# Kernel optimization log

Hardware: AMD Instinct MI355X
Metric: run time of the kernel (lower is better)

## Reference

```python
import jax, jax.numpy as jnp
import numpy as np

N = 50000   # nodes
E = 800000  # edges (avg degree 16)
H = 8       # num_heads
D = 16      # head_dim = hidden_size // num_heads = 128 // 8


def setup_inputs() -> dict:
    key = jax.random.key(0)
    k1, k2, k3, k4, k5 = jax.random.split(key, 5)
    q = jax.random.normal(k1, (N, D, H), dtype=jnp.float32)
    k = jax.random.normal(k2, (N, D, H), dtype=jnp.float32)
    v = jax.random.normal(k3, (N, D, H), dtype=jnp.float32)
    # COO adjacency: row = destination node of each edge, col = source node
    row = jnp.sort(jax.random.randint(k4, (E,), 0, N, dtype=jnp.int32))
    col = jax.random.randint(k5, (E,), 0, N, dtype=jnp.int32)
    return {"q": q, "k": k, "v": v, "row": row, "col": col}


def reference(q, k, v, row, col):
    # bsddmm: sampled dense-dense matmul -> per-edge, per-head attention logits
    # logits[e, h] = sum_d q[row[e], d, h] * k[col[e], d, h]
    logits = jnp.einsum('edh,edh->eh', q[row], k[col])  # [E, H]

    # sparse softmax over each destination row (per head), numerically stable
    m = jax.ops.segment_max(logits, row, num_segments=N)  # [N, H]
    p = jnp.exp(logits - m[row])                          # [E, H]
    s = jax.ops.segment_sum(p, row, num_segments=N)       # [N, H]
    attn = p / s[row]                                     # [E, H]

    # bspmm: out[i, d, h] = sum_{e: row[e]==i} attn[e, h] * v[col[e], d, h]
    out = jax.ops.segment_sum(attn[:, None, :] * v[col], row, num_segments=N)  # [N, D, H]
    return out.reshape(N, -1)  # [N, D*H]
```

## Files before the change

### kernel.cpp

```cpp
#include <hip/hip_runtime.h>
#include <math.h>

#define HEADS 8
#define DIM 16
#define NPB 32

__global__ __launch_bounds__(256) void spmha_kernel(
    const float* __restrict__ q, const float* __restrict__ k, const float* __restrict__ v,
    const int* __restrict__ row, const int* __restrict__ col,
    float* __restrict__ out, int N, int E) {
  __shared__ int rp[NPB + 1];

  int node0 = blockIdx.x * NPB;

  if (threadIdx.x <= NPB) {
    int target = node0 + threadIdx.x;
    int lo = 0, hi = E;
    while (lo < hi) {
      int mid = (lo + hi) >> 1;
      if (row[mid] < target) lo = mid + 1; else hi = mid;
    }
    rp[threadIdx.x] = lo;
  }
  __syncthreads();

  int il = threadIdx.x >> 3;
  int i  = node0 + il;
  int l  = threadIdx.x & 7;
  bool alive = (i < N);

  int s = alive ? rp[il] : 0;
  int e = alive ? rp[il + 1] : 0;

  float qv[16];
  if (alive) {
    const float4* qb = (const float4*)(q + (size_t)i * 128);
#pragma unroll
    for (int r = 0; r < 4; ++r) *(float4*)&qv[4 * r] = qb[8 * r + l];
  }

  float o[16];
#pragma unroll
  for (int x = 0; x < 16; ++x) o[x] = 0.f;
  float m[4], den[4];
#pragma unroll
  for (int j = 0; j < 4; ++j) { m[j] = -INFINITY; den[j] = 0.f; }

  auto do_edge = [&](const float* kk, const float* vv) {
    float part[4];
#pragma unroll
    for (int j = 0; j < 4; ++j) part[j] = 0.f;
#pragma unroll
    for (int r = 0; r < 4; ++r)
#pragma unroll
      for (int j = 0; j < 4; ++j)
        part[j] = fmaf(qv[4 * r + j], kk[4 * r + j], part[j]);
#pragma unroll
    for (int j = 0; j < 4; ++j) {
      part[j] += __shfl_xor(part[j], 2);
      part[j] += __shfl_xor(part[j], 4);
    }
#pragma unroll
    for (int j = 0; j < 4; ++j) {
      float mn = fmaxf(m[j], part[j]);
      float sc = __expf(m[j] - mn);
      float p  = __expf(part[j] - mn);
      den[j] = fmaf(den[j], sc, p);
      m[j] = mn;
#pragma unroll
      for (int r = 0; r < 4; ++r)
        o[4 * r + j] = fmaf(o[4 * r + j], sc, p * vv[4 * r + j]);
    }
  };

  int eidx = s;
  for (; eidx + 2 <= e; eidx += 2) {
    int c0 = col[eidx];
    int c1 = col[eidx + 1];
    const float4* kb0 = (const float4*)(k + (size_t)c0 * 128);
    const float4* vb0 = (const float4*)(v + (size_t)c0 * 128);
    const float4* kb1 = (const float4*)(k + (size_t)c1 * 128);
    const float4* vb1 = (const float4*)(v + (size_t)c1 * 128);
    float kk0[16], vv0[16], kk1[16], vv1[16];
#pragma unroll
    for (int r = 0; r < 4; ++r) {
      *(float4*)&kk0[4 * r] = kb0[8 * r + l];
      *(float4*)&vv0[4 * r] = vb0[8 * r + l];
      *(float4*)&kk1[4 * r] = kb1[8 * r + l];
      *(float4*)&vv1[4 * r] = vb1[8 * r + l];
    }
    do_edge(kk0, vv0);
    do_edge(kk1, vv1);
  }
  if (eidx < e) {
    int c0 = col[eidx];
    const float4* kb0 = (const float4*)(k + (size_t)c0 * 128);
    const float4* vb0 = (const float4*)(v + (size_t)c0 * 128);
    float kk0[16], vv0[16];
#pragma unroll
    for (int r = 0; r < 4; ++r) {
      *(float4*)&kk0[4 * r] = kb0[8 * r + l];
      *(float4*)&vv0[4 * r] = vb0[8 * r + l];
    }
    do_edge(kk0, vv0);
  }

  if (alive) {
    float inv[4];
#pragma unroll
    for (int j = 0; j < 4; ++j) inv[j] = (e > s) ? 1.f / den[j] : 0.f;
    float4* ob = (float4*)(out + (size_t)i * 128);
#pragma unroll
    for (int r = 0; r < 4; ++r) {
      float4 res;
      res.x = o[4 * r + 0] * inv[0];
      res.y = o[4 * r + 1] * inv[1];
      res.z = o[4 * r + 2] * inv[2];
      res.w = o[4 * r + 3] * inv[3];
      ob[8 * r + l] = res;
    }
  }
}

extern "C" void kernel_launch(void* const* d_in, const int* in_sizes, int n_in,
                              void* d_out, int out_size, void* d_ws, size_t ws_size,
                              hipStream_t stream) {
  const float* q   = (const float*)d_in[0];
  const float* k   = (const float*)d_in[1];
  const float* v   = (const float*)d_in[2];
  const int*   row = (const int*)d_in[3];
  const int*   col = (const int*)d_in[4];
  float* out = (float*)d_out;

  int N = in_sizes[0] / (DIM * HEADS);
  int E = in_sizes[3];

  int total = N * HEADS;
  int grid = (total + 255) / 256;
  spmha_kernel<<<grid, 256, 0, stream>>>(q, k, v, row, col, out, N, E);
}
```

Baseline: 231.5 us.

## Convert K and V to interleaved bf16 workspace before gathering per-edge rows

Adds a pre-pass that rounds K and V to bf16 and packs each node's K and V rows together into a workspace buffer. The main kernel then gathers half as many bytes per edge, in one contiguous 512-byte row, and also changes which lanes own which head and dim elements. This targets the random-gather memory traffic that dominates the kernel, at the cost of an extra conversion pass over K and V and reduced precision in logits and outputs. It falls back to the fp32 kernel when the workspace is too small.

```diff
diff --git a/kernel.cpp b/kernel.cpp
--- a/kernel.cpp
+++ b/kernel.cpp
@@ -5,14 +5,37 @@
 #define DIM 16
 #define NPB 32
 
-__global__ __launch_bounds__(256) void spmha_kernel(
-    const float* __restrict__ q, const float* __restrict__ k, const float* __restrict__ v,
+static __device__ __forceinline__ unsigned short f2bf(float f) {
+  unsigned u = __float_as_uint(f);
+  u += 0x7FFFu + ((u >> 16) & 1u);
+  return (unsigned short)(u >> 16);
+}
+static __device__ __forceinline__ float bflo(unsigned u) { return __uint_as_float(u << 16); }
+static __device__ __forceinline__ float bfhi(unsigned u) { return __uint_as_float(u & 0xFFFF0000u); }
+
+__global__ __launch_bounds__(256) void conv_kernel(
+    const float* __restrict__ k, const float* __restrict__ v,
+    unsigned short* __restrict__ kv, int N) {
+  int j = blockIdx.x * blockDim.x + threadIdx.x;
+  if (j >= N * 32) return;
+  int i = j >> 5, c = j & 31;
+  const float* src = (c < 16 ? k : v) + (size_t)i * 128 + (c & 15) * 8;
+  float4 f0 = ((const float4*)src)[0];
+  float4 f1 = ((const float4*)src)[1];
+  uint4 r;
+  r.x = (unsigned)f2bf(f0.x) | ((unsigned)f2bf(f0.y) << 16);
+  r.y = (unsigned)f2bf(f0.z) | ((unsigned)f2bf(f0.w) << 16);
+  r.z = (unsigned)f2bf(f1.x) | ((unsigned)f2bf(f1.y) << 16);
+  r.w = (unsigned)f2bf(f1.z) | ((unsigned)f2bf(f1.w) << 16);
+  *(uint4*)(kv + (size_t)i * 256 + c * 8) = r;
+}
+
+__global__ __launch_bounds__(256) void spmha_bf16_kernel(
+    const float* __restrict__ q, const unsigned short* __restrict__ kv,
     const int* __restrict__ row, const int* __restrict__ col,
     float* __restrict__ out, int N, int E) {
   __shared__ int rp[NPB + 1];
-
   int node0 = blockIdx.x * NPB;
-
   if (threadIdx.x <= NPB) {
     int target = node0 + threadIdx.x;
     int lo = 0, hi = E;
@@ -28,17 +51,115 @@
   int i  = node0 + il;
   int l  = threadIdx.x & 7;
   bool alive = (i < N);
-
   int s = alive ? rp[il] : 0;
   int e = alive ? rp[il + 1] : 0;
 
+  float qv0[8], qv1[8];
+  if (alive) {
+    const float4* qp = (const float4*)(q + (size_t)i * 128);
+    *(float4*)&qv0[0] = qp[2 * l];
+    *(float4*)&qv0[4] = qp[2 * l + 1];
+    *(float4*)&qv1[0] = qp[16 + 2 * l];
+    *(float4*)&qv1[4] = qp[16 + 2 * l + 1];
+  }
+
+  float o0[8], o1[8], m[8], den[8];
+#pragma unroll
+  for (int h = 0; h < 8; ++h) { o0[h] = 0.f; o1[h] = 0.f; m[h] = -INFINITY; den[h] = 0.f; }
+
+  auto cvt8 = [](const uint4& A, float* f) {
+    f[0] = bflo(A.x); f[1] = bfhi(A.x); f[2] = bflo(A.y); f[3] = bfhi(A.y);
+    f[4] = bflo(A.z); f[5] = bfhi(A.z); f[6] = bflo(A.w); f[7] = bfhi(A.w);
+  };
+
+  auto do_edge = [&](const uint4& A, const uint4& B, const uint4& C, const uint4& D) {
+    float kf0[8], kf1[8], vf0[8], vf1[8];
+    cvt8(A, kf0); cvt8(B, kf1); cvt8(C, vf0); cvt8(D, vf1);
+    float part[8];
+#pragma unroll
+    for (int h = 0; h < 8; ++h) part[h] = fmaf(qv0[h], kf0[h], qv1[h] * kf1[h]);
+#pragma unroll
+    for (int h = 0; h < 8; ++h) part[h] += __shfl_xor(part[h], 1);
+#pragma unroll
+    for (int h = 0; h < 8; ++h) part[h] += __shfl_xor(part[h], 2);
+#pragma unroll
+    for (int h = 0; h < 8; ++h) part[h] += __shfl_xor(part[h], 4);
+#pragma unroll
+    for (int h = 0; h < 8; ++h) {
+      float mn = fmaxf(m[h], part[h]);
+      float sc = __expf(m[h] - mn);
+      float p  = __expf(part[h] - mn);
+      den[h] = fmaf(den[h], sc, p);
+      m[h] = mn;
+      o0[h] = fmaf(o0[h], sc, p * vf0[h]);
+      o1[h] = fmaf(o1[h], sc, p * vf1[h]);
+    }
+  };
+
+  int eidx = s;
+  for (; eidx + 2 <= e; eidx += 2) {
+    int c0 = col[eidx];
+    int c1 = col[eidx + 1];
+    const uint4* b0 = (const uint4*)(kv + (size_t)c0 * 256);
+    const uint4* b1 = (const uint4*)(kv + (size_t)c1 * 256);
+    uint4 A0 = b0[l], B0 = b0[8 + l], C0 = b0[16 + l], D0 = b0[24 + l];
+    uint4 A1 = b1[l], B1 = b1[8 + l], C1 = b1[16 + l], D1 = b1[24 + l];
+    do_edge(A0, B0, C0, D0);
+    do_edge(A1, B1, C1, D1);
+  }
+  if (eidx < e) {
+    int c0 = col[eidx];
+    const uint4* b0 = (const uint4*)(kv + (size_t)c0 * 256);
+    do_edge(b0[l], b0[8 + l], b0[16 + l], b0[24 + l]);
+  }
+
+  if (alive) {
+    float inv[8];
+#pragma unroll
+    for (int h = 0; h < 8; ++h) inv[h] = (e > s) ? 1.f / den[h] : 0.f;
+    float4* op = (float4*)(out + (size_t)i * 128);
+    float4 r;
+    r.x = o0[0] * inv[0]; r.y = o0[1] * inv[1]; r.z = o0[2] * inv[2]; r.w = o0[3] * inv[3];
+    op[2 * l] = r;
+    r.x = o0[4] * inv[4]; r.y = o0[5] * inv[5]; r.z = o0[6] * inv[6]; r.w = o0[7] * inv[7];
+    op[2 * l + 1] = r;
+    r.x = o1[0] * inv[0]; r.y = o1[1] * inv[1]; r.z = o1[2] * inv[2]; r.w = o1[3] * inv[3];
+    op[16 + 2 * l] = r;
+    r.x = o1[4] * inv[4]; r.y = o1[5] * inv[5]; r.z = o1[6] * inv[6]; r.w = o1[7] * inv[7];
+    op[16 + 2 * l + 1] = r;
+  }
+}
+
+__global__ __launch_bounds__(256) void spmha_f32_kernel(
+    const float* __restrict__ q, const float* __restrict__ k, const float* __restrict__ v,
+    const int* __restrict__ row, const int* __restrict__ col,
+    float* __restrict__ out, int N, int E) {
+  __shared__ int rp[NPB + 1];
+  int node0 = blockIdx.x * NPB;
+  if (threadIdx.x <= NPB) {
+    int target = node0 + threadIdx.x;
+    int lo = 0, hi = E;
+    while (lo < hi) {
+      int mid = (lo + hi) >> 1;
+      if (row[mid] < target) lo = mid + 1; else hi = mid;
+    }
+    rp[threadIdx.x] = lo;
+  }
+  __syncthreads();
+
+  int il = threadIdx.x >> 3;
+  int i  = node0 + il;
+  int l  = threadIdx.x & 7;
+  bool alive = (i < N);
+  int s = alive ? rp[il] : 0;
+  int e = alive ? rp[il + 1] : 0;
+
   float qv[16];
   if (alive) {
     const float4* qb = (const float4*)(q + (size_t)i * 128);
 #pragma unroll
     for (int r = 0; r < 4; ++r) *(float4*)&qv[4 * r] = qb[8 * r + l];
   }
-
   float o[16];
 #pragma unroll
   for (int x = 0; x < 16; ++x) o[x] = 0.f;
@@ -74,25 +195,7 @@
   };
 
   int eidx = s;
-  for (; eidx + 2 <= e; eidx += 2) {
-    int c0 = col[eidx];
-    int c1 = col[eidx + 1];
-    const float4* kb0 = (const float4*)(k + (size_t)c0 * 128);
-    const float4* vb0 = (const float4*)(v + (size_t)c0 * 128);
-    const float4* kb1 = (const float4*)(k + (size_t)c1 * 128);
-    const float4* vb1 = (const float4*)(v + (size_t)c1 * 128);
-    float kk0[16], vv0[16], kk1[16], vv1[16];
-#pragma unroll
-    for (int r = 0; r < 4; ++r) {
-      *(float4*)&kk0[4 * r] = kb0[8 * r + l];
-      *(float4*)&vv0[4 * r] = vb0[8 * r + l];
-      *(float4*)&kk1[4 * r] = kb1[8 * r + l];
-      *(float4*)&vv1[4 * r] = vb1[8 * r + l];
-    }
-    do_edge(kk0, vv0);
-    do_edge(kk1, vv1);
-  }
-  if (eidx < e) {
+  for (; eidx < e; ++eidx) {
     int c0 = col[eidx];
     const float4* kb0 = (const float4*)(k + (size_t)c0 * 128);
     const float4* vb0 = (const float4*)(v + (size_t)c0 * 128);
@@ -135,7 +238,16 @@
   int N = in_sizes[0] / (DIM * HEADS);
   int E = in_sizes[3];
 
+  size_t kv_bytes = (size_t)N * 512;
   int total = N * HEADS;
   int grid = (total + 255) / 256;
-  spmha_kernel<<<grid, 256, 0, stream>>>(q, k, v, row, col, out, N, E);
-}
+
+  if (ws_size >= kv_bytes) {
+    unsigned short* kv = (unsigned short*)d_ws;
+    int cgrid = (N * 32 + 255) / 256;
+    conv_kernel<<<cgrid, 256, 0, stream>>>(k, v, kv, N);
+    spmha_bf16_kernel<<<grid, 256, 0, stream>>>(q, kv, row, col, out, N, E);
+  } else {
+    spmha_f32_kernel<<<grid, 256, 0, stream>>>(q, k, v, row, col, out, N, E);
+  }
+}
```

After: 239.8 us. 1.04x slower.
